# Kernel optimization log

Hardware: AMD Instinct MI355X
Metric: run time of the kernel (lower is better)

The kernel has to match this reference:

```python
import jax, jax.numpy as jnp
import numpy as np

MARGIN = 1.0
EPS = 1e-8  # torch F.cosine_similarity default eps


def setup_inputs() -> dict:
    key = jax.random.key(0)
    k1, k2 = jax.random.split(key)
    reps = jax.random.normal(k1, (8192, 512), dtype=jnp.float32)
    labels = jax.random.randint(k2, (8192,), 0, 100, dtype=jnp.int64)
    return {"reps": reps, "labels": labels}


def reference(reps, labels):
    # cosine_similarity(reps[None, :, :], reps[:, None, :], dim=2)
    # == dot(a,b) / (max(||a||,eps) * max(||b||,eps)); compute via normalize + GEMM
    norms = jnp.maximum(jnp.linalg.norm(reps, axis=1, keepdims=True), EPS)
    xn = reps / norms  # [N, D]
    cos_sim = xn @ xn.T  # [N, N]
    label_matrix = labels[None, :] == labels[:, None]  # [N, N] bool
    same_class_loss = jnp.where(label_matrix, (1.0 - cos_sim) ** 2, 0.0)
    diff_class_loss = jnp.where(label_matrix, 0.0,
                                jnp.maximum(MARGIN - cos_sim, 0.0) ** 2)
    loss = same_class_loss + diff_class_loss
    return loss.mean()
```

## Files before the change

kernel.cpp:

```cpp
#include <hip/hip_runtime.h>


typedef __attribute__((ext_vector_type(8))) short  s8;
typedef __attribute__((ext_vector_type(8))) __bf16 bf8;
typedef __attribute__((ext_vector_type(4))) float  f4;
typedef __attribute__((ext_vector_type(4))) unsigned short u4v;

#define NT32 136
#define KOUT 16
#define KCW  512
#define GSTRIDE (256 * 512)

#define OFF_XT  0u
#define OFF_INV (8u * 1024u * 1024u)
#define OFF_S   (OFF_INV + 8192u * 4u)
#define OFF_S2  (OFF_S + 512u * 4u)
#define OFF_TK  (OFF_S2 + 4u)
#define OFF_GP  (OFF_S2 + 64u)

__device__ __forceinline__ unsigned short f2bf(float f) {
    union { float f; unsigned u; } v; v.f = f;
    unsigned r = v.u + 0x7FFFu + ((v.u >> 16) & 1u);
    return (unsigned short)(r >> 16);
}

__global__ __launch_bounds__(256) void k_norms(
    const float* __restrict__ reps, float* __restrict__ inv,
    float* __restrict__ zbuf )
{
    const int t = threadIdx.x, lane = t & 63, w = t >> 6;
    if (blockIdx.x == 0) {
        for (int z = t; z < 514; z += 256) zbuf[z] = 0.f;
    }
    const int row = blockIdx.x * 4 + w;
    const float4 x0 = *(const float4*)(reps + (size_t)row * 512 + lane * 4);
    const float4 x1 = *(const float4*)(reps + (size_t)row * 512 + 256 + lane * 4);
    float ss = x0.x*x0.x + x0.y*x0.y + x0.z*x0.z + x0.w*x0.w
             + x1.x*x1.x + x1.y*x1.y + x1.z*x1.z + x1.w*x1.w;
    #pragma unroll
    for (int off = 1; off < 64; off <<= 1) ss += __shfl_xor(ss, off, 64);
    if (lane == 0) inv[row] = 1.0f / fmaxf(sqrtf(ss), 1e-8f);
}

__global__ __launch_bounds__(256) void k_norm_transpose(
    const float* __restrict__ reps, const float* __restrict__ inv,
    unsigned short* __restrict__ xt, float* __restrict__ svec)
{
    __shared__ unsigned short tile[64][72];
    __shared__ float sred[4][64];
    const int t = threadIdx.x, lane = t & 63, w = t >> 6;
    const int a0 = blockIdx.x * 64, i0 = blockIdx.y * 64;
    const int colg = t & 15;
    const int ig0  = t >> 4;

    float4 sa = {0.f, 0.f, 0.f, 0.f};
    #pragma unroll
    for (int j = 0; j < 4; ++j) {
        const int il = ig0 + j * 16;
        const float iv = inv[i0 + il];
        const float4 x = *(const float4*)(reps + (size_t)(i0 + il) * 512 + a0 + colg * 4);
        const float4 xn = {x.x * iv, x.y * iv, x.z * iv, x.w * iv};
        sa.x += xn.x; sa.y += xn.y; sa.z += xn.z; sa.w += xn.w;
        ushort4 p;
        p.x = f2bf(xn.x); p.y = f2bf(xn.y); p.z = f2bf(xn.z); p.w = f2bf(xn.w);
        *(ushort4*)&tile[il][colg * 4] = p;
    }
    __syncthreads();

    {
        const int ig = t & 15, ag = t >> 4;
        u4v rows[4];
        #pragma unroll
        for (int r = 0; r < 4; ++r)
            rows[r] = *(const u4v*)&tile[ig * 4 + r][ag * 4];
        const int gbase = a0 >> 4;
        const int c     = (i0 >> 5) + (ig >> 3);
        const int ks    = (ig >> 1) & 3;
        const int ke4   = ig & 1;
        #pragma unroll
        for (int j = 0; j < 4; ++j) {
            const int al = ag * 4 + j;
            const int g  = gbase + (al >> 4);
            const int rl = al & 15;
            ushort4 o;
            o.x = (unsigned short)rows[0][j];
            o.y = (unsigned short)rows[1][j];
            o.z = (unsigned short)rows[2][j];
            o.w = (unsigned short)rows[3][j];
            *(ushort4*)(xt + ((((size_t)g * 256 + c) << 9)
                              + (ks * 16 + rl) * 8 + ke4 * 4)) = o;
        }
    }

    sa.x += __shfl_xor(sa.x, 16, 64); sa.x += __shfl_xor(sa.x, 32, 64);
    sa.y += __shfl_xor(sa.y, 16, 64); sa.y += __shfl_xor(sa.y, 32, 64);
    sa.z += __shfl_xor(sa.z, 16, 64); sa.z += __shfl_xor(sa.z, 32, 64);
    sa.w += __shfl_xor(sa.w, 16, 64); sa.w += __shfl_xor(sa.w, 32, 64);
    if (lane < 16) {
        sred[w][lane * 4 + 0] = sa.x; sred[w][lane * 4 + 1] = sa.y;
        sred[w][lane * 4 + 2] = sa.z; sred[w][lane * 4 + 3] = sa.w;
    }
    __syncthreads();
    if (t < 64) {
        const float v = sred[0][t] + sred[1][t] + sred[2][t] + sred[3][t];
        atomicAdd(&svec[a0 + t], v);
    }
}

__global__ __launch_bounds__(64) void k_gram(
    const unsigned short* __restrict__ xt, float* __restrict__ gp)
{
    const int lane = threadIdx.x;
    const int l15 = lane & 15, l4 = lane >> 4;
    int tt = blockIdx.x, ta = 0;
    while (tt >= 16 - ta) { tt -= 16 - ta; ++ta; }
    const int tb = ta + tt;
    const int c0 = blockIdx.y * (KCW / 32);
    const unsigned short* A0 = xt + (((size_t)(ta * 2) * 256 + c0) << 9) + lane * 8;
    const unsigned short* B0 = xt + (((size_t)(tb * 2) * 256 + c0) << 9) + lane * 8;

    f4 acc00 = {0.f,0.f,0.f,0.f}, acc01 = {0.f,0.f,0.f,0.f};
    f4 acc10 = {0.f,0.f,0.f,0.f}, acc11 = {0.f,0.f,0.f,0.f};

    if (ta != tb) {
        for (int cc = 0; cc < 16; ++cc) {
            const s8 av0 = *(const s8*)(A0 + cc * 512);
            const s8 av1 = *(const s8*)(A0 + GSTRIDE + cc * 512);
            const s8 bv0 = *(const s8*)(B0 + cc * 512);
            const s8 bv1 = *(const s8*)(B0 + GSTRIDE + cc * 512);
            acc00 = __builtin_amdgcn_mfma_f32_16x16x32_bf16(
                __builtin_bit_cast(bf8, av0), __builtin_bit_cast(bf8, bv0), acc00, 0, 0, 0);
            acc01 = __builtin_amdgcn_mfma_f32_16x16x32_bf16(
                __builtin_bit_cast(bf8, av0), __builtin_bit_cast(bf8, bv1), acc01, 0, 0, 0);
            acc10 = __builtin_amdgcn_mfma_f32_16x16x32_bf16(
                __builtin_bit_cast(bf8, av1), __builtin_bit_cast(bf8, bv0), acc10, 0, 0, 0);
            acc11 = __builtin_amdgcn_mfma_f32_16x16x32_bf16(
                __builtin_bit_cast(bf8, av1), __builtin_bit_cast(bf8, bv1), acc11, 0, 0, 0);
        }
    } else {
        for (int cc = 0; cc < 16; ++cc) {
            const s8 av0 = *(const s8*)(A0 + cc * 512);
            const s8 av1 = *(const s8*)(A0 + GSTRIDE + cc * 512);
            acc00 = __builtin_amdgcn_mfma_f32_16x16x32_bf16(
                __builtin_bit_cast(bf8, av0), __builtin_bit_cast(bf8, av0), acc00, 0, 0, 0);
            acc01 = __builtin_amdgcn_mfma_f32_16x16x32_bf16(
                __builtin_bit_cast(bf8, av0), __builtin_bit_cast(bf8, av1), acc01, 0, 0, 0);
            acc10 = __builtin_amdgcn_mfma_f32_16x16x32_bf16(
                __builtin_bit_cast(bf8, av1), __builtin_bit_cast(bf8, av0), acc10, 0, 0, 0);
            acc11 = __builtin_amdgcn_mfma_f32_16x16x32_bf16(
                __builtin_bit_cast(bf8, av1), __builtin_bit_cast(bf8, av1), acc11, 0, 0, 0);
        }
    }

    float* gb = gp + ((size_t)blockIdx.y * NT32 + blockIdx.x) * 1024;
    #pragma unroll
    for (int r = 0; r < 4; ++r) {
        const int ar0 = (l4 * 4 + r) * 32 + l15;
        gb[ar0]           = acc00[r];
        gb[ar0 + 16]      = acc01[r];
        gb[ar0 + 16 * 32] = acc10[r];
        gb[ar0 + 16 * 33] = acc11[r];
    }
}

__global__ __launch_bounds__(256) void k_reduce_final(
    const float* __restrict__ gp, const float* __restrict__ svec,
    float* __restrict__ s2, int* __restrict__ ticket,
    float* __restrict__ out)
{
    __shared__ float part[4];
    __shared__ int lastFlag;
    const int t = threadIdx.x;
    const int c = blockIdx.x * 256 + t;
    const f4* g4 = (const f4*)gp;
    f4 s = {0.f, 0.f, 0.f, 0.f};
    #pragma unroll
    for (int p = 0; p < KOUT; ++p) s += g4[(size_t)p * (NT32 * 256) + c];
    int tt = c >> 8, ta = 0;
    while (tt >= 16 - ta) { tt -= 16 - ta; ++ta; }
    const float wgt = (tt == 0) ? 1.f : 2.f;
    float sq = wgt * (s.x * s.x + s.y * s.y + s.z * s.z + s.w * s.w);
    #pragma unroll
    for (int off = 1; off < 64; off <<= 1) sq += __shfl_xor(sq, off, 64);
    if ((t & 63) == 0) part[t >> 6] = sq;
    __syncthreads();
    if (t == 0) {
        atomicAdd(s2, part[0] + part[1] + part[2] + part[3]);
        __threadfence();
        lastFlag = (atomicAdd(ticket, 1) == (int)gridDim.x - 1);
    }
    __syncthreads();
    if (lastFlag) {
        __threadfence();
        const float v0 = svec[t], v1 = svec[t + 256];
        float p = v0 * v0 + v1 * v1;
        #pragma unroll
        for (int off = 1; off < 64; off <<= 1) p += __shfl_xor(p, off, 64);
        if ((t & 63) == 0) part[t >> 6] = p;
        __syncthreads();
        if (t == 0) {
            const float s1 = part[0] + part[1] + part[2] + part[3];
            const float S2 = atomicAdd(s2, 0.f);
            const double NN = 67108864.0;
            out[0] = (float)((NN - 2.0 * (double)s1 + (double)S2) / NN);
        }
    }
}

extern "C" void kernel_launch(void* const* d_in, const int* in_sizes, int n_in,
                              void* d_out, int out_size, void* d_ws, size_t ws_size,
                              hipStream_t stream)
{
    const float* reps = (const float*)d_in[0];
    char* ws = (char*)d_ws;
    unsigned short* xt   = (unsigned short*)(ws + OFF_XT);
    float*          invn = (float*)(ws + OFF_INV);
    float*          svec = (float*)(ws + OFF_S);
    float*          s2   = (float*)(ws + OFF_S2);
    int*            tick = (int*)(ws + OFF_TK);
    float*          gp   = (float*)(ws + OFF_GP);

    k_norms<<<2048, 256, 0, stream>>>(reps, invn, svec);
    k_norm_transpose<<<dim3(8, 128), 256, 0, stream>>>(reps, invn, xt, svec);
    k_gram<<<dim3(NT32, KOUT), 64, 0, stream>>>(xt, gp);
    k_reduce_final<<<NT32, 256, 0, stream>>>(gp, svec, s2, tick, (float*)d_out);
}
```

Baseline: 91.40 us.

## Fuse norm and transpose kernels into one prep pass with per-block column sums

Merges the row-norm kernel and the normalize/transpose kernel into a single k_prep kernel. Each block loads 32 full rows once, computes the norms in registers, and writes the bf16 transposed layout from shared memory. Column sums are now written as per-block partials instead of global atomics, and the final reduce kernel folds the s1 term into its atomic accumulator. This removes one launch and a second read of reps, at the cost of fewer blocks (256) and strided partial reads in the reduce.

```diff
diff --git a/kernel.cpp b/kernel.cpp
--- a/kernel.cpp
+++ b/kernel.cpp
@@ -4,7 +4,6 @@
 typedef __attribute__((ext_vector_type(8))) short  s8;
 typedef __attribute__((ext_vector_type(8))) __bf16 bf8;
 typedef __attribute__((ext_vector_type(4))) float  f4;
-typedef __attribute__((ext_vector_type(4))) unsigned short u4v;
 
 #define NT32 136
 #define KOUT 16
@@ -12,98 +11,79 @@
 #define GSTRIDE (256 * 512)
 
 #define OFF_XT  0u
-#define OFF_INV (8u * 1024u * 1024u)
-#define OFF_S   (OFF_INV + 8192u * 4u)
-#define OFF_S2  (OFF_S + 512u * 4u)
+#define OFF_S2  (8u * 1024u * 1024u)
 #define OFF_TK  (OFF_S2 + 4u)
-#define OFF_GP  (OFF_S2 + 64u)
+#define OFF_PRT (OFF_S2 + 64u)
+#define OFF_GP  (OFF_PRT + 256u * 512u * 4u)
 
 __device__ __forceinline__ unsigned short f2bf(float f) {
     union { float f; unsigned u; } v; v.f = f;
     unsigned r = v.u + 0x7FFFu + ((v.u >> 16) & 1u);
     return (unsigned short)(r >> 16);
 }
-
-__global__ __launch_bounds__(256) void k_norms(
-    const float* __restrict__ reps, float* __restrict__ inv,
-    float* __restrict__ zbuf )
-{
-    const int t = threadIdx.x, lane = t & 63, w = t >> 6;
-    if (blockIdx.x == 0) {
-        for (int z = t; z < 514; z += 256) zbuf[z] = 0.f;
-    }
-    const int row = blockIdx.x * 4 + w;
-    const float4 x0 = *(const float4*)(reps + (size_t)row * 512 + lane * 4);
-    const float4 x1 = *(const float4*)(reps + (size_t)row * 512 + 256 + lane * 4);
-    float ss = x0.x*x0.x + x0.y*x0.y + x0.z*x0.z + x0.w*x0.w
-             + x1.x*x1.x + x1.y*x1.y + x1.z*x1.z + x1.w*x1.w;
-    #pragma unroll
-    for (int off = 1; off < 64; off <<= 1) ss += __shfl_xor(ss, off, 64);
-    if (lane == 0) inv[row] = 1.0f / fmaxf(sqrtf(ss), 1e-8f);
-}
-
-__global__ __launch_bounds__(256) void k_norm_transpose(
-    const float* __restrict__ reps, const float* __restrict__ inv,
-    unsigned short* __restrict__ xt, float* __restrict__ svec)
-{
-    __shared__ unsigned short tile[64][72];
-    __shared__ float sred[4][64];
-    const int t = threadIdx.x, lane = t & 63, w = t >> 6;
-    const int a0 = blockIdx.x * 64, i0 = blockIdx.y * 64;
-    const int colg = t & 15;
-    const int ig0  = t >> 4;
-
-    float4 sa = {0.f, 0.f, 0.f, 0.f};
-    #pragma unroll
-    for (int j = 0; j < 4; ++j) {
-        const int il = ig0 + j * 16;
-        const float iv = inv[i0 + il];
-        const float4 x = *(const float4*)(reps + (size_t)(i0 + il) * 512 + a0 + colg * 4);
-        const float4 xn = {x.x * iv, x.y * iv, x.z * iv, x.w * iv};
-        sa.x += xn.x; sa.y += xn.y; sa.z += xn.z; sa.w += xn.w;
+__device__ __forceinline__ float bf2f(unsigned short h) {
+    union { unsigned u; float f; } v; v.u = ((unsigned)h) << 16;
+    return v.f;
+}
+
+__global__ __launch_bounds__(256) void k_prep(
+    const float* __restrict__ reps, unsigned short* __restrict__ xt,
+    float* __restrict__ parts, float* __restrict__ s2, int* __restrict__ ticket)
+{
+    __shared__ unsigned short tile[32][528];
+    const int t = threadIdx.x, lane = t & 63, wv = t >> 6;
+    const int b = blockIdx.x;
+    if (b == 0 && t == 0) { *s2 = 0.f; *ticket = 0; }
+
+    const int row = wv * 8 + (lane >> 3);
+    const int co  = (lane & 7) * 4;
+    const float* rp = reps + (size_t)(b * 32 + row) * 512 + co;
+    float4 v[16];
+    float ss = 0.f;
+    #pragma unroll
+    for (int q = 0; q < 16; ++q) {
+        v[q] = *(const float4*)(rp + 32 * q);
+        ss += v[q].x*v[q].x + v[q].y*v[q].y + v[q].z*v[q].z + v[q].w*v[q].w;
+    }
+    ss += __shfl_xor(ss, 1, 64);
+    ss += __shfl_xor(ss, 2, 64);
+    ss += __shfl_xor(ss, 4, 64);
+    const float inv = 1.0f / fmaxf(sqrtf(ss), 1e-8f);
+    #pragma unroll
+    for (int q = 0; q < 16; ++q) {
         ushort4 p;
-        p.x = f2bf(xn.x); p.y = f2bf(xn.y); p.z = f2bf(xn.z); p.w = f2bf(xn.w);
-        *(ushort4*)&tile[il][colg * 4] = p;
+        p.x = f2bf(v[q].x * inv); p.y = f2bf(v[q].y * inv);
+        p.z = f2bf(v[q].z * inv); p.w = f2bf(v[q].w * inv);
+        *(ushort4*)&tile[row][co + 32 * q] = p;
     }
     __syncthreads();
 
     {
-        const int ig = t & 15, ag = t >> 4;
-        u4v rows[4];
-        #pragma unroll
-        for (int r = 0; r < 4; ++r)
-            rows[r] = *(const u4v*)&tile[ig * 4 + r][ag * 4];
-        const int gbase = a0 >> 4;
-        const int c     = (i0 >> 5) + (ig >> 3);
-        const int ks    = (ig >> 1) & 3;
-        const int ke4   = ig & 1;
-        #pragma unroll
-        for (int j = 0; j < 4; ++j) {
-            const int al = ag * 4 + j;
-            const int g  = gbase + (al >> 4);
-            const int rl = al & 15;
-            ushort4 o;
-            o.x = (unsigned short)rows[0][j];
-            o.y = (unsigned short)rows[1][j];
-            o.z = (unsigned short)rows[2][j];
-            o.w = (unsigned short)rows[3][j];
-            *(ushort4*)(xt + ((((size_t)g * 256 + c) << 9)
-                              + (ks * 16 + rl) * 8 + ke4 * 4)) = o;
-        }
-    }
-
-    sa.x += __shfl_xor(sa.x, 16, 64); sa.x += __shfl_xor(sa.x, 32, 64);
-    sa.y += __shfl_xor(sa.y, 16, 64); sa.y += __shfl_xor(sa.y, 32, 64);
-    sa.z += __shfl_xor(sa.z, 16, 64); sa.z += __shfl_xor(sa.z, 32, 64);
-    sa.w += __shfl_xor(sa.w, 16, 64); sa.w += __shfl_xor(sa.w, 32, 64);
-    if (lane < 16) {
-        sred[w][lane * 4 + 0] = sa.x; sred[w][lane * 4 + 1] = sa.y;
-        sred[w][lane * 4 + 2] = sa.z; sred[w][lane * 4 + 3] = sa.w;
-    }
-    __syncthreads();
-    if (t < 64) {
-        const float v = sred[0][t] + sred[1][t] + sred[2][t] + sred[3][t];
-        atomicAdd(&svec[a0 + t], v);
+        const int rl = lane & 15, ks = lane >> 4;
+        #pragma unroll
+        for (int gg = 0; gg < 8; ++gg) {
+            const int g = wv * 8 + gg;
+            const int a = g * 16 + rl;
+            ushort4 o0, o1;
+            o0.x = tile[ks*8+0][a]; o0.y = tile[ks*8+1][a];
+            o0.z = tile[ks*8+2][a]; o0.w = tile[ks*8+3][a];
+            o1.x = tile[ks*8+4][a]; o1.y = tile[ks*8+5][a];
+            o1.z = tile[ks*8+6][a]; o1.w = tile[ks*8+7][a];
+            unsigned short* dst = xt + ((size_t)g << 17) + ((size_t)b << 9) + lane * 8;
+            *(ushort4*)(dst)     = o0;
+            *(ushort4*)(dst + 4) = o1;
+        }
+    }
+
+    {
+        float sA = 0.f, sB = 0.f;
+        #pragma unroll
+        for (int r = 0; r < 32; ++r) {
+            sA += bf2f(tile[r][t]);
+            sB += bf2f(tile[r][t + 256]);
+        }
+        parts[(size_t)b * 512 + t]       = sA;
+        parts[(size_t)b * 512 + t + 256] = sB;
     }
 }
 
@@ -164,13 +144,12 @@
 }
 
 __global__ __launch_bounds__(256) void k_reduce_final(
-    const float* __restrict__ gp, const float* __restrict__ svec,
-    float* __restrict__ s2, int* __restrict__ ticket,
-    float* __restrict__ out)
-{
-    __shared__ float part[4];
+    const float* __restrict__ gp, const float* __restrict__ parts,
+    float* __restrict__ s2, int* __restrict__ ticket, float* __restrict__ out)
+{
+    __shared__ float part[4], svp[4];
     __shared__ int lastFlag;
-    const int t = threadIdx.x;
+    const int t = threadIdx.x, lane = t & 63, wv = t >> 6;
     const int c = blockIdx.x * 256 + t;
     const f4* g4 = (const f4*)gp;
     f4 s = {0.f, 0.f, 0.f, 0.f};
@@ -182,27 +161,32 @@
     float sq = wgt * (s.x * s.x + s.y * s.y + s.z * s.z + s.w * s.w);
     #pragma unroll
     for (int off = 1; off < 64; off <<= 1) sq += __shfl_xor(sq, off, 64);
-    if ((t & 63) == 0) part[t >> 6] = sq;
+    if (lane == 0) part[wv] = sq;
+
+    float sv = 0.f;
+    if (blockIdx.x < 128) {
+        const int a = blockIdx.x * 4 + wv;
+        #pragma unroll
+        for (int pb = 0; pb < 4; ++pb) sv += parts[(size_t)(pb * 64 + lane) * 512 + a];
+        #pragma unroll
+        for (int off = 1; off < 64; off <<= 1) sv += __shfl_xor(sv, off, 64);
+    }
+    if (lane == 0) svp[wv] = sv;
     __syncthreads();
     if (t == 0) {
-        atomicAdd(s2, part[0] + part[1] + part[2] + part[3]);
+        const float tot = part[0] + part[1] + part[2] + part[3]
+            - 2.f * (svp[0]*svp[0] + svp[1]*svp[1] + svp[2]*svp[2] + svp[3]*svp[3]);
+        atomicAdd(s2, tot);
         __threadfence();
         lastFlag = (atomicAdd(ticket, 1) == (int)gridDim.x - 1);
     }
     __syncthreads();
     if (lastFlag) {
         __threadfence();
-        const float v0 = svec[t], v1 = svec[t + 256];
-        float p = v0 * v0 + v1 * v1;
-        #pragma unroll
-        for (int off = 1; off < 64; off <<= 1) p += __shfl_xor(p, off, 64);
-        if ((t & 63) == 0) part[t >> 6] = p;
-        __syncthreads();
         if (t == 0) {
-            const float s1 = part[0] + part[1] + part[2] + part[3];
-            const float S2 = atomicAdd(s2, 0.f);
+            const float S = atomicAdd(s2, 0.f);
             const double NN = 67108864.0;
-            out[0] = (float)((NN - 2.0 * (double)s1 + (double)S2) / NN);
+            out[0] = (float)((NN + (double)S) / NN);
         }
     }
 }
@@ -214,14 +198,12 @@
     const float* reps = (const float*)d_in[0];
     char* ws = (char*)d_ws;
     unsigned short* xt   = (unsigned short*)(ws + OFF_XT);
-    float*          invn = (float*)(ws + OFF_INV);
-    float*          svec = (float*)(ws + OFF_S);
     float*          s2   = (float*)(ws + OFF_S2);
     int*            tick = (int*)(ws + OFF_TK);
+    float*          prt  = (float*)(ws + OFF_PRT);
     float*          gp   = (float*)(ws + OFF_GP);
 
-    k_norms<<<2048, 256, 0, stream>>>(reps, invn, svec);
-    k_norm_transpose<<<dim3(8, 128), 256, 0, stream>>>(reps, invn, xt, svec);
+    k_prep<<<256, 256, 0, stream>>>(reps, xt, prt, s2, tick);
     k_gram<<<dim3(NT32, KOUT), 64, 0, stream>>>(xt, gp);
-    k_reduce_final<<<NT32, 256, 0, stream>>>(gp, svec, s2, tick, (float*)d_out);
-}
+    k_reduce_final<<<NT32, 256, 0, stream>>>(gp, prt, s2, tick, (float*)d_out);
+}
```

After: 87.33 us. -4.5%, faster.
